# Kernel optimization log

Hardware: AMD Instinct MI355X
Metric: run time of the kernel (lower is better)

Reference implementation:

```python
import jax, jax.numpy as jnp
import numpy as np

# Mamba2(d_model=256, headdim=32) defaults: d_state=128, d_conv=4, expand=2, ngroups=1, chunk=256
B, CIN, L = 8, 256, 1024
D_MODEL = CIN
D_INNER = 2 * D_MODEL            # expand=2 -> 512
HEADDIM = 32
NHEADS = D_INNER // HEADDIM      # 16
D_STATE = 128
D_CONV = 4
CONV_DIM = D_INNER + 2 * D_STATE             # 768 (ngroups=1)
D_IN_PROJ = 2 * D_INNER + 2 * D_STATE + NHEADS  # 1296
GN_GROUPS = 8
CHUNK = 256
EPS = 1e-5

def setup_inputs():
    key = jax.random.key(0)
    ks = jax.random.split(key, 8)
    x = jax.random.normal(ks[0], (B, CIN, L), jnp.float32)
    W_in = jax.random.normal(ks[1], (D_IN_PROJ, D_MODEL), jnp.float32) * 0.02
    conv_w = jax.random.normal(ks[2], (CONV_DIM, D_CONV), jnp.float32) * 0.2
    conv_b = jax.random.normal(ks[3], (CONV_DIM,), jnp.float32) * 0.02
    dt = jnp.exp(jax.random.uniform(ks[4], (NHEADS,)) * (jnp.log(0.1) - jnp.log(0.001)) + jnp.log(0.001))
    dt_bias = dt + jnp.log(-jnp.expm1(-dt))   # inverse softplus
    A_log = jnp.log(jax.random.uniform(ks[5], (NHEADS,), minval=1.0, maxval=16.0))
    Dp = jnp.ones((NHEADS,), jnp.float32)
    rms_w = jnp.ones((D_INNER,), jnp.float32)
    W_out = jax.random.normal(ks[6], (D_MODEL, D_INNER), jnp.float32) * 0.02
    gn_w = jnp.ones((CIN,), jnp.float32)
    gn_b = jnp.zeros((CIN,), jnp.float32)
    return dict(x=x, W_in=W_in, conv_w=conv_w, conv_b=conv_b, dt_bias=dt_bias,
                A_log=A_log, Dp=Dp, rms_w=rms_w, W_out=W_out, gn_w=gn_w, gn_b=gn_b)

def segsum(a):
    # a: (..., T) -> (..., T, T) with sum_{j<i<=t} a_i on/below diagonal, -inf above
    T = a.shape[-1]
    cs = jnp.cumsum(a, -1)
    d = cs[..., :, None] - cs[..., None, :]
    mask = jnp.tril(jnp.ones((T, T), bool))
    return jnp.where(mask, d, -jnp.inf)

def ssd(X, A, Bm, Cm):
    # X: (b,l,h,p) already dt-scaled; A: (b,l,h) = dt*A_cont; Bm,Cm: (b,l,n) (ngroups=1)
    b, l, h, p = X.shape
    n = Bm.shape[-1]
    c = l // CHUNK
    X = X.reshape(b, c, CHUNK, h, p)
    A = A.reshape(b, c, CHUNK, h).transpose(0, 3, 1, 2)      # (b,h,c,l)
    Bm = Bm.reshape(b, c, CHUNK, n)
    Cm = Cm.reshape(b, c, CHUNK, n)
    A_cs = jnp.cumsum(A, -1)                                  # (b,h,c,l)
    Lmat = jnp.exp(segsum(A))                                 # (b,h,c,l,l)
    Y_diag = jnp.einsum('bcln,bcsn,bhcls,bcshp->bclhp', Cm, Bm, Lmat, X)
    decay_states = jnp.exp(A_cs[..., -1:] - A_cs)             # (b,h,c,l)
    states = jnp.einsum('bcln,bhcl,bclhp->bchpn', Bm, decay_states, X)
    decay_chunk = jnp.exp(segsum(jnp.pad(A_cs[..., -1], ((0, 0), (0, 0), (1, 0)))))  # (b,h,c+1,c+1)
    states = jnp.concatenate([jnp.zeros_like(states[:, :1]), states], axis=1)        # (b,c+1,h,p,n)
    prev = jnp.einsum('bhzc,bchpn->bzhpn', decay_chunk, states)[:, :-1]              # (b,c,h,p,n)
    Y_off = jnp.einsum('bcln,bchpn,bhcl->bclhp', Cm, prev, jnp.exp(A_cs))
    return (Y_diag + Y_off).reshape(b, l, h, p)

def _forward(x, W_in, conv_w, conv_b, dt_bias, A_log, Dp, rms_w, W_out, gn_w, gn_b):
    u = jnp.transpose(x, (0, 2, 1))                           # (B,L,d_model)
    zxbcdt = u @ W_in.T                                       # (B,L,1296)
    z = zxbcdt[..., :D_INNER]
    xBC = zxbcdt[..., D_INNER:D_INNER + CONV_DIM]
    dt = jax.nn.softplus(zxbcdt[..., D_INNER + CONV_DIM:] + dt_bias)  # (B,L,H)
    # causal depthwise conv1d + SiLU
    xpad = jnp.pad(xBC, ((0, 0), (D_CONV - 1, 0), (0, 0)))
    xconv = conv_b + sum(conv_w[:, k] * xpad[:, k:k + L, :] for k in range(D_CONV))
    xconv = jax.nn.silu(xconv)
    xs = xconv[..., :D_INNER].reshape(B, L, NHEADS, HEADDIM)
    Bm = xconv[..., D_INNER:D_INNER + D_STATE]
    Cm = xconv[..., D_INNER + D_STATE:]
    A = -jnp.exp(A_log)                                       # (H,)
    Y = ssd(dt[..., None] * xs, dt * A, Bm, Cm)               # (B,L,H,P)
    Y = Y + xs * Dp[None, None, :, None]
    # gated RMSNorm (norm_before_gate=False): rmsnorm(y * silu(z)) * weight
    y = Y.reshape(B, L, D_INNER) * jax.nn.silu(z)
    y = y * jax.lax.rsqrt(jnp.mean(y * y, -1, keepdims=True) + EPS) * rms_w
    out = jnp.transpose(y @ W_out.T, (0, 2, 1))               # (B,C,L)
    # GroupNorm(8, C) over (channels_per_group, L)
    og = out.reshape(B, GN_GROUPS, CIN // GN_GROUPS, L)
    mu = og.mean((2, 3), keepdims=True)
    var = og.var((2, 3), keepdims=True)
    out = ((og - mu) * jax.lax.rsqrt(var + EPS)).reshape(B, CIN, L)
    out = out * gn_w[None, :, None] + gn_b[None, :, None]
    return out * jnp.tanh(jax.nn.softplus(out))               # Mish

def reference(x, W_in, conv_w, conv_b, dt_bias, A_log, Dp, rms_w, W_out, gn_w, gn_b):
    return _forward(x, W_in, conv_w, conv_b, dt_bias, A_log, Dp, rms_w, W_out, gn_w, gn_b)
```

## Files before the change

kernel.cpp:

```cpp
#include <hip/hip_runtime.h>
#include <hip/hip_bf16.h>
#include <math.h>

#define B_ 8
#define L_ 1024
#define DM 256
#define DI 512
#define HD 32
#define NH 16
#define DS 128
#define CDIM 768
#define NZX 1280
#define CH 256
#define NC 4
#define M_ (B_*L_)
#define EPSV 1e-5f

typedef short bf16x8 __attribute__((ext_vector_type(8)));
typedef float f32x4 __attribute__((ext_vector_type(4)));

#define OFF_ZX   0
#define SZ_ZX    (M_*NZX/2)
#define OFF_XC   (OFF_ZX+SZ_ZX)
#define SZ_XC    (M_*CDIM/2)
#define OFF_DTP  (OFF_XC+SZ_XC)
#define SZ_DTP   (4*M_*NH)
#define OFF_ACS  (OFF_DTP+SZ_DTP)
#define SZ_ACS   (B_*NC*NH*CH)
#define OFF_S0   (OFF_ACS+SZ_ACS)
#define SZ_S0    (B_*NC*CH*CH/2)
#define OFF_ST   (OFF_S0+SZ_S0)
#define SZ_ST    (B_*NC*NH*HD*DS/2)
#define OFF_Y    (OFF_ST+SZ_ST)
#define SZ_Y     (M_*DI/2)
#define OFF_YNB  (OFF_Y+SZ_Y)
#define SZ_YNB   (M_*DI/2)
#define OFF_XBF  (OFF_YNB+SZ_YNB)
#define SZ_XBF   (M_*DM/2)
#define OFF_WBF  (OFF_XBF+SZ_XBF)
#define SZ_WBF   (1296*DM/2)
#define OFF_WOBF (OFF_WBF+SZ_WBF)
#define SZ_WOBF  (DM*DI/2)
#define OFF_GNP  (OFF_WOBF+SZ_WOBF)
#define SZ_GNP   (64*2)
#define OFF_BT   (OFF_GNP+SZ_GNP)
#define SZ_BT    (32*128*256/2)
#define OFF_OUTB (OFF_BT+SZ_BT)
#define SZ_OUTB  (M_*DM/2)

__device__ __forceinline__ ushort f2bf(float v) {
  __hip_bfloat16 h = __float2bfloat16(v);
  return *(ushort*)&h;
}
__device__ __forceinline__ float bf2f(ushort u) {
  return __uint_as_float(((unsigned int)u) << 16);
}
__device__ __forceinline__ float dt_load(const float* __restrict__ dtp, size_t di) {
  float s = dtp[di] + dtp[(size_t)M_*NH + di] + dtp[2*(size_t)M_*NH + di] + dtp[3*(size_t)M_*NH + di];
  return (s > 20.f) ? s : log1pf(expf(s));
}

__device__ __forceinline__ void gload16(const ushort* g, ushort* l) {
  __builtin_amdgcn_global_load_lds(
      (const __attribute__((address_space(1))) unsigned int*)g,
      (__attribute__((address_space(3))) unsigned int*)l,
      16, 0, 0);
}

__global__ __launch_bounds__(256) void k_prep(const float* __restrict__ x,
                                              const float* __restrict__ W_in,
                                              const float* __restrict__ W_out,
                                              const float* __restrict__ dt_bias,
                                              ushort* __restrict__ xbf,
                                              ushort* __restrict__ wbf,
                                              ushort* __restrict__ wobf,
                                              float2* __restrict__ gnp,
                                              float* __restrict__ dtp) {
  __shared__ float Ts[64][65];
  __shared__ float Wd[16][65];
  const int bid = blockIdx.x;
  const int t = threadIdx.x;
  if (bid < 512) {
    const int kt = bid & 3, lt2 = (bid >> 2) & 15, b = bid >> 6;
    const int k0 = kt*64, l0 = lt2*64;
    for (int i = t; i < 1024; i += 256) {
      int kk = i>>4, lw = i&15;
      float4 v = *(const float4*)&x[(size_t)b*DM*L_ + (size_t)(k0+kk)*L_ + l0 + lw*4];
      Ts[kk][lw*4+0] = v.x; Ts[kk][lw*4+1] = v.y;
      Ts[kk][lw*4+2] = v.z; Ts[kk][lw*4+3] = v.w;
    }
    for (int i = t; i < 1024; i += 256) {
      int h = i>>6, kk = i&63;
      Wd[h][kk] = W_in[(size_t)(NZX+h)*DM + k0+kk];
    }
    __syncthreads();
    for (int i = t; i < 512; i += 256) {
      int mm = i>>3, kg = i&7;
      union { ushort u[8]; uint4 q; } pk;
#pragma unroll
      for (int j = 0; j < 8; ++j) pk.u[j] = f2bf(Ts[kg*8+j][mm]);
      *(uint4*)&xbf[(size_t)(b*L_ + l0+mm)*DM + k0 + kg*8] = pk.q;
    }
    const int h = t&15, lg = t>>4;
    const float bias = (kt == 0) ? dt_bias[h] : 0.f;
#pragma unroll
    for (int c = 0; c < 4; ++c) {
      const int ll = lg + c*16;
      float acc = bias;
#pragma unroll 8
      for (int kk = 0; kk < 64; ++kk) acc += Wd[h][kk]*Ts[kk][ll];
      dtp[(size_t)kt*M_*NH + (size_t)(b*L_ + l0+ll)*NH + h] = acc;
    }
  } else if (bid < 512 + 1296) {
    int i = (bid-512)*256 + t;
    if (i < 1296*DM) wbf[i] = f2bf(W_in[i]);
  } else if (bid < 512 + 1296 + 512) {
    int i = (bid-512-1296)*256 + t;
    wobf[i] = f2bf(W_out[i]);
  } else {
    if (t < 64) gnp[t] = make_float2(0.f, 0.f);
  }
}

__global__ __launch_bounds__(256) void k_gemm_in_mfma(const ushort* __restrict__ xbf,
                                                      const ushort* __restrict__ wbf,
                                                      ushort* __restrict__ zxb) {
  __shared__ __attribute__((aligned(16))) ushort As[2][128*32];
  __shared__ __attribute__((aligned(16))) ushort Bs[2][128*32];
  const int tid = threadIdx.x;
  const int n0 = blockIdx.x*128, m0 = blockIdx.y*128;
  const int wave = tid>>6, lane = tid&63;
  const int lr = lane&15, quad = lane>>4;
  const int rA = lane>>2;
  const int cA = (lane&3)*8;
  f32x4 acc[2][8];
#pragma unroll
  for (int mi=0;mi<2;++mi)
#pragma unroll
    for (int ni=0;ni<8;++ni)
#pragma unroll
      for (int r=0;r<4;++r) acc[mi][ni][r] = 0.f;
  auto STAGE = [&](int buf, int k0) {
#pragma unroll
    for (int j = 0; j < 2; ++j) {
      const int ch = 2*wave + j;
      const int row = ch*16 + rA;
      gload16(xbf + (size_t)(m0+row)*DM + k0 + cA, &As[buf][ch*512]);
      gload16(wbf + (size_t)(n0+row)*DM + k0 + cA, &Bs[buf][ch*512]);
    }
  };
  STAGE(0, 0);
#pragma unroll
  for (int i = 0; i < 8; ++i) {
    __syncthreads();
    if (i < 7) STAGE((i+1)&1, (i+1)*32);
    const int cur = i&1;
    bf16x8 af[2], bfr[8];
    af[0] = *(const bf16x8*)&As[cur][(wave*32+lr)*32 + quad*8];
    af[1] = *(const bf16x8*)&As[cur][(wave*32+16+lr)*32 + quad*8];
#pragma unroll
    for (int ni=0;ni<8;++ni) bfr[ni] = *(const bf16x8*)&Bs[cur][(ni*16+lr)*32 + quad*8];
#pragma unroll
    for (int mi=0;mi<2;++mi)
#pragma unroll
      for (int ni=0;ni<8;++ni)
        acc[mi][ni] = __builtin_amdgcn_mfma_f32_16x16x32_bf16(af[mi], bfr[ni], acc[mi][ni], 0, 0, 0);
  }
#pragma unroll
  for (int mi=0;mi<2;++mi) {
    int m = m0 + wave*32 + mi*16 + quad*4;
#pragma unroll
    for (int ni=0;ni<8;++ni) {
      int n = n0 + ni*16 + lr;
#pragma unroll
      for (int r=0;r<4;++r) zxb[(size_t)(m+r)*NZX + n] = f2bf(acc[mi][ni][r]);
    }
  }
}

__global__ __launch_bounds__(256) void k_conv(const ushort* __restrict__ zxb,
                                              const float* __restrict__ cw,
                                              const float* __restrict__ cb,
                                              ushort* __restrict__ xcb,
                                              ushort* __restrict__ btg) {
  const int j = blockIdx.x*256 + threadIdx.x;
  const int m8 = blockIdx.y*8;
  const int l0 = m8 & 1023;
  const int mb = m8 & ~1023;
  const float4 w = *(const float4*)&cw[j*4];
  const float bias = cb[j];
  float v[11];
#pragma unroll
  for (int i = 0; i < 11; ++i) {
    int ll = l0 - 3 + i;
    v[i] = (ll >= 0) ? bf2f(zxb[(size_t)(mb+ll)*NZX + DI + j]) : 0.f;
  }
  union { ushort u[8]; uint4 q; } res;
#pragma unroll
  for (int i = 0; i < 8; ++i) {
    float a = bias + w.x*v[i] + w.y*v[i+1] + w.z*v[i+2] + w.w*v[i+3];
    a = a / (1.f + expf(-a));
    res.u[i] = f2bf(a);
    xcb[(size_t)(mb+l0+i)*CDIM + j] = res.u[i];
  }
  if (j >= DI && j < DI+DS) {
    const int n = j - DI;
    const int bc = (mb >> 10)*NC + (l0 >> 8);
    const int lc = l0 & 255;
    *(uint4*)&btg[((size_t)bc*DS + n)*CH + lc] = res.q;
  }
}

__global__ __launch_bounds__(256) void k_s0st(const ushort* __restrict__ xcb,
                                              const ushort* __restrict__ btg,
                                              const float* __restrict__ dtp,
                                              const float* __restrict__ A_log,
                                              float* __restrict__ acs_g,
                                              ushort* __restrict__ stb,
                                              ushort* __restrict__ S0b) {
  __shared__ float wtot[4];
  __shared__ ushort Xw[32][264];
  const int role = blockIdx.x;
  const int bc = blockIdx.y;
  const int base = bc*CH;
  const int t = threadIdx.x;
  const int wave = t>>6, lane = t&63, lr = lane&15, quad = lane>>4;
  if (role < 10) {
    const int lt = (role>=6) ? 3 : (role>=3) ? 2 : (role>=1) ? 1 : 0;
    const int st = role - lt*(lt+1)/2;
    const int l = lt*64 + wave*16 + lr;
    f32x4 acc[4];
#pragma unroll
    for (int nt = 0; nt < 4; ++nt)
#pragma unroll
      for (int r = 0; r < 4; ++r) acc[nt][r] = 0.f;
#pragma unroll
    for (int ks = 0; ks < 4; ++ks) {
      bf16x8 af = *(const bf16x8*)(xcb + (size_t)(base+l)*CDIM + (DI+DS) + ks*32 + quad*8);
#pragma unroll
      for (int nt = 0; nt < 4; ++nt) {
        bf16x8 bf = *(const bf16x8*)(xcb + (size_t)(base + st*64 + nt*16 + lr)*CDIM + DI + ks*32 + quad*8);
        acc[nt] = __builtin_amdgcn_mfma_f32_16x16x32_bf16(af, bf, acc[nt], 0, 0, 0);
      }
    }
    const bool diag = (lt == st);
#pragma unroll
    for (int nt = 0; nt < 4; ++nt)
#pragma unroll
      for (int r = 0; r < 4; ++r) {
        const int lrow = lt*64 + wave*16 + quad*4 + r;
        const int scol = st*64 + nt*16 + lr;
        ushort v = (!diag || scol <= lrow) ? f2bf(acc[nt][r]) : (ushort)0;
        S0b[((size_t)bc*CH + lrow)*CH + scol] = v;
      }
    return;
  }
  const int h = role - 10;
  float dt_t = dt_load(dtp, (size_t)(base+t)*NH + h);
  float An = -expf(A_log[h]);
  float v = dt_t * An;
#pragma unroll
  for (int off = 1; off < 64; off <<= 1) {
    float u = __shfl_up(v, off);
    if (lane >= off) v += u;
  }
  if (lane == 63) wtot[wave] = v;
  __syncthreads();
  float pre = 0.f, tot = 0.f;
#pragma unroll
  for (int wj = 0; wj < 4; ++wj) {
    float wv = wtot[wj];
    tot += wv;
    if (wj < wave) pre += wv;
  }
  const float a = v + pre;
  const float alast = tot;
  acs_g[((size_t)bc*NH + h)*CH + t] = a;
  float w = expf(alast - a) * dt_t;
  {
    const ushort* xp = xcb + (size_t)(base+t)*CDIM + h*HD;
    ushort tmp[32];
    *(uint4*)&tmp[0]  = *(const uint4*)(xp);
    *(uint4*)&tmp[8]  = *(const uint4*)(xp+8);
    *(uint4*)&tmp[16] = *(const uint4*)(xp+16);
    *(uint4*)&tmp[24] = *(const uint4*)(xp+24);
#pragma unroll
    for (int p = 0; p < 32; ++p) Xw[p][t] = f2bf(bf2f(tmp[p]) * w);
  }
  __syncthreads();
  f32x4 acc2[2][2];
#pragma unroll
  for (int mt=0;mt<2;++mt)
#pragma unroll
    for (int nt=0;nt<2;++nt)
#pragma unroll
      for (int r=0;r<4;++r) acc2[mt][nt][r] = 0.f;
  const ushort* bp = btg + (size_t)bc*DS*CH;
#pragma unroll
  for (int k0 = 0; k0 < CH; k0 += 32) {
    bf16x8 a0 = *(const bf16x8*)&Xw[lr][k0 + quad*8];
    bf16x8 a1 = *(const bf16x8*)&Xw[16+lr][k0 + quad*8];
    bf16x8 b0 = *(const bf16x8*)(bp + (size_t)(wave*32 + lr)*CH + k0 + quad*8);
    bf16x8 b1 = *(const bf16x8*)(bp + (size_t)(wave*32 + 16 + lr)*CH + k0 + quad*8);
    acc2[0][0] = __builtin_amdgcn_mfma_f32_16x16x32_bf16(a0, b0, acc2[0][0], 0,0,0);
    acc2[0][1] = __builtin_amdgcn_mfma_f32_16x16x32_bf16(a0, b1, acc2[0][1], 0,0,0);
    acc2[1][0] = __builtin_amdgcn_mfma_f32_16x16x32_bf16(a1, b0, acc2[1][0], 0,0,0);
    acc2[1][1] = __builtin_amdgcn_mfma_f32_16x16x32_bf16(a1, b1, acc2[1][1], 0,0,0);
  }
  size_t sb = ((size_t)bc*NH + h)*HD*DS;
#pragma unroll
  for (int mt = 0; mt < 2; ++mt)
#pragma unroll
    for (int nt = 0; nt < 2; ++nt)
#pragma unroll
      for (int r = 0; r < 4; ++r)
        stb[sb + (size_t)(mt*16 + quad*4 + r)*DS + wave*32 + nt*16 + lr] = f2bf(acc2[mt][nt][r]);
}

__global__ __launch_bounds__(256) void k_y_mfma(const ushort* __restrict__ xcb,
    const float* __restrict__ dtp, const float* __restrict__ acs_g,
    const ushort* __restrict__ S0b, const ushort* __restrict__ stb,
    const float* __restrict__ Dp, ushort* __restrict__ Yb) {
  __shared__ ushort Xt[32][280];
  __shared__ ushort Xs[32][280];
  __shared__ float acs[CH];
  const int t = threadIdx.x;
  const int bc = blockIdx.x, h = blockIdx.y;
  const int base = bc*CH;
  const int cc = bc & 3, bc4 = bc & ~3;
  acs[t] = acs_g[((size_t)bc*NH + h)*CH + t];
  const float dts_t = dt_load(dtp, (size_t)(base+t)*NH + h);
  ushort tmp[32];
  {
    const ushort* xp = xcb + (size_t)(base+t)*CDIM + h*HD;
    *(uint4*)&tmp[0]  = *(const uint4*)(xp);
    *(uint4*)&tmp[8]  = *(const uint4*)(xp+8);
    *(uint4*)&tmp[16] = *(const uint4*)(xp+16);
    *(uint4*)&tmp[24] = *(const uint4*)(xp+24);
#pragma unroll
    for (int p = 0; p < 32; ++p) Xt[p][t] = tmp[p];
  }
  __syncthreads();
  const float e32 = expf(acs[t & ~31] - acs[t]) * dts_t;
#pragma unroll
  for (int p = 0; p < 32; ++p) Xs[p][t] = f2bf(bf2f(tmp[p]) * e32);
  __syncthreads();
  const int wave = t>>6, lane = t&63, lr = lane&15, quad = lane>>4;
  f32x4 acc[4][2];
#pragma unroll
  for (int mt=0;mt<4;++mt)
#pragma unroll
    for (int nt=0;nt<2;++nt)
#pragma unroll
      for (int r=0;r<4;++r) acc[mt][nt][r] = 0.f;
  if (cc > 0) {
    float fj[3];
    {
      float cum = 0.f;
      for (int j = cc-1; j >= 0; --j) {
        fj[j] = expf(cum);
        cum += acs_g[((size_t)(bc4+j)*NH + h)*CH + (CH-1)];
      }
    }
#pragma unroll
    for (int ks = 0; ks < 4; ++ks) {
      bf16x8 bfr[2];
#pragma unroll
      for (int nt = 0; nt < 2; ++nt) {
        float P[8];
#pragma unroll
        for (int jj = 0; jj < 8; ++jj) P[jj] = 0.f;
        for (int j = 0; j < cc; ++j) {
          bf16x8 sv = *(const bf16x8*)(stb + ((size_t)(bc4+j)*NH + h)*HD*DS
                                       + (size_t)(nt*16+lr)*DS + ks*32 + quad*8);
#pragma unroll
          for (int jj = 0; jj < 8; ++jj) P[jj] += fj[j]*bf2f((ushort)sv[jj]);
        }
        bf16x8 bb;
#pragma unroll
        for (int jj = 0; jj < 8; ++jj) bb[jj] = (short)f2bf(P[jj]);
        bfr[nt] = bb;
      }
#pragma unroll
      for (int mt = 0; mt < 4; ++mt) {
        int l = mt*64 + wave*16 + lr;
        bf16x8 af = *(const bf16x8*)(xcb + (size_t)(base+l)*CDIM + (DI+DS) + ks*32 + quad*8);
        acc[mt][0] = __builtin_amdgcn_mfma_f32_16x16x32_bf16(af, bfr[0], acc[mt][0], 0,0,0);
        acc[mt][1] = __builtin_amdgcn_mfma_f32_16x16x32_bf16(af, bfr[1], acc[mt][1], 0,0,0);
      }
    }
    const float es0 = expf(acs[0]);
#pragma unroll
    for (int mt = 0; mt < 4; ++mt)
#pragma unroll
      for (int nt = 0; nt < 2; ++nt)
#pragma unroll
        for (int r = 0; r < 4; ++r) acc[mt][nt][r] *= es0;
  }
  const int Kw = (12 + wave) >> 1;
  for (int ks = 0; ks <= Kw; ++ks) {
    const int sq = ks*32;
    const bf16x8 xb0 = *(const bf16x8*)&Xs[lr][sq + quad*8];
    const bf16x8 xb1 = *(const bf16x8*)&Xs[16+lr][sq + quad*8];
    const float g = (ks > 0) ? expf(acs[sq] - acs[sq-32]) : 1.f;
#pragma unroll
    for (int mt = 0; mt < 4; ++mt) {
      const int rt = 4*mt + wave;
      if (ks > (rt>>1)) continue;
      if (ks > 0) {
#pragma unroll
        for (int r = 0; r < 4; ++r) { acc[mt][0][r] *= g; acc[mt][1][r] *= g; }
      }
      const int l = mt*64 + wave*16 + lr;
      const bf16x8 sb = *(const bf16x8*)(S0b + ((size_t)bc*CH + l)*CH + sq + quad*8);
      acc[mt][0] = __builtin_amdgcn_mfma_f32_16x16x32_bf16(sb, xb0, acc[mt][0], 0,0,0);
      acc[mt][1] = __builtin_amdgcn_mfma_f32_16x16x32_bf16(sb, xb1, acc[mt][1], 0,0,0);
    }
  }
  const float dph = Dp[h];
#pragma unroll
  for (int mt = 0; mt < 4; ++mt) {
    const int Kmt = (4*mt + wave) >> 1;
    const float aref = acs[32*Kmt];
    const int lb = mt*64 + wave*16 + quad*4;
#pragma unroll
    for (int r = 0; r < 4; ++r) {
      const float e = expf(acs[lb+r] - aref);
#pragma unroll
      for (int nt = 0; nt < 2; ++nt) {
        const int p = nt*16 + lr;
        float xv = bf2f(Xt[p][lb+r]);
        Yb[(size_t)(base+lb+r)*DI + h*HD + p] = f2bf(acc[mt][nt][r]*e + dph*xv);
      }
    }
  }
}

__global__ __launch_bounds__(256) void k_rms(const ushort* __restrict__ zxb,
                                             const ushort* __restrict__ Yb,
                                             const float* __restrict__ rw,
                                             ushort* __restrict__ yn) {
  const int m = blockIdx.x*4 + (threadIdx.x>>6);
  const int lane = threadIdx.x & 63;
  const int c0 = lane*8;
  bf16x8 zv = *(const bf16x8*)(zxb + (size_t)m*NZX + c0);
  bf16x8 yv = *(const bf16x8*)(Yb  + (size_t)m*DI  + c0);
  float y[8];
  float ss = 0.f;
#pragma unroll
  for (int j = 0; j < 8; ++j) {
    float z = bf2f((ushort)zv[j]);
    y[j] = bf2f((ushort)yv[j]) * z / (1.f + expf(-z));
    ss += y[j]*y[j];
  }
#pragma unroll
  for (int off = 1; off < 64; off <<= 1) ss += __shfl_xor(ss, off);
  const float inv = rsqrtf(ss * (1.f/DI) + EPSV);
  float4 w0 = *(const float4*)&rw[c0];
  float4 w1 = *(const float4*)&rw[c0+4];
  const float wv[8] = {w0.x,w0.y,w0.z,w0.w,w1.x,w1.y,w1.z,w1.w};
  union { ushort u[8]; uint4 q; } pk;
#pragma unroll
  for (int j = 0; j < 8; ++j) pk.u[j] = f2bf(y[j] * inv * wv[j]);
  *(uint4*)(yn + (size_t)m*DI + c0) = pk.q;
}

__global__ __launch_bounds__(256) void k_gemm_out_mfma(const ushort* __restrict__ ynbf,
                                                       const ushort* __restrict__ wobf,
                                                       ushort* __restrict__ outb,
                                                       float2* __restrict__ gnp) {
  __shared__ __attribute__((aligned(16))) ushort As[2][64*32];
  __shared__ __attribute__((aligned(16))) ushort Bs[2][128*32];
  __shared__ float red[4][8];
  const int tid = threadIdx.x;
  const int n0 = blockIdx.x*128, m0 = blockIdx.y*64;
  const int wave = tid>>6, lane = tid&63;
  const int lr = lane&15, quad = lane>>4;
  const int rA = lane>>2;
  const int cA = (lane&3)*8;
  f32x4 acc[8];
#pragma unroll
  for (int ni=0;ni<8;++ni)
#pragma unroll
    for (int r=0;r<4;++r) acc[ni][r] = 0.f;
  auto STAGE = [&](int buf, int k0) {
    gload16(ynbf + (size_t)(m0 + wave*16 + rA)*DI + k0 + cA, &As[buf][wave*512]);
#pragma unroll
    for (int j = 0; j < 2; ++j) {
      const int ch = 2*wave + j;
      gload16(wobf + (size_t)(n0 + ch*16 + rA)*DI + k0 + cA, &Bs[buf][ch*512]);
    }
  };
  STAGE(0, 0);
#pragma unroll
  for (int i = 0; i < 16; ++i) {
    __syncthreads();
    if (i < 15) STAGE((i+1)&1, (i+1)*32);
    const int cur = i&1;
    bf16x8 af = *(const bf16x8*)&As[cur][(wave*16+lr)*32 + quad*8];
    bf16x8 bfr[8];
#pragma unroll
    for (int ni=0;ni<8;++ni) bfr[ni] = *(const bf16x8*)&Bs[cur][(ni*16+lr)*32 + quad*8];
#pragma unroll
    for (int ni=0;ni<8;++ni)
      acc[ni] = __builtin_amdgcn_mfma_f32_16x16x32_bf16(af, bfr[ni], acc[ni], 0, 0, 0);
  }
  const int b = m0 >> 10, l0 = m0 & 1023;
  float sg[4] = {0.f,0.f,0.f,0.f}, sq2[4] = {0.f,0.f,0.f,0.f};
#pragma unroll
  for (int ni=0;ni<8;++ni) {
    int n = n0 + ni*16 + lr;
    union { ushort u[4]; uint2 q; } pk;
#pragma unroll
    for (int r=0;r<4;++r) pk.u[r] = f2bf(acc[ni][r]);
    *(uint2*)&outb[(size_t)b*DM*L_ + (size_t)n*L_ + l0 + wave*16 + quad*4] = pk.q;
    float ps = acc[ni][0]+acc[ni][1]+acc[ni][2]+acc[ni][3];
    float pq = acc[ni][0]*acc[ni][0]+acc[ni][1]*acc[ni][1]
             + acc[ni][2]*acc[ni][2]+acc[ni][3]*acc[ni][3];
    sg[ni>>1] += ps; sq2[ni>>1] += pq;
  }
#pragma unroll
  for (int g = 0; g < 4; ++g)
#pragma unroll
    for (int off = 32; off > 0; off >>= 1) {
      sg[g]  += __shfl_down(sg[g],  off);
      sq2[g] += __shfl_down(sq2[g], off);
    }
  if (lane == 0) {
#pragma unroll
    for (int g = 0; g < 4; ++g) { red[wave][g] = sg[g]; red[wave][4+g] = sq2[g]; }
  }
  __syncthreads();
  if (tid == 0) {
    int g0 = b*8 + (n0>>5);
#pragma unroll
    for (int g = 0; g < 4; ++g) {
      float S = red[0][g]+red[1][g]+red[2][g]+red[3][g];
      float Q = red[0][4+g]+red[1][4+g]+red[2][4+g]+red[3][4+g];
      atomicAdd(&gnp[g0+g].x, S);
      atomicAdd(&gnp[g0+g].y, Q);
    }
  }
}

__global__ __launch_bounds__(256) void k_gn_apply(const float2* __restrict__ gnp,
                                                  const float* __restrict__ gw,
                                                  const float* __restrict__ gb,
                                                  const ushort* __restrict__ ob,
                                                  float* __restrict__ o) {
  const int ch = blockIdx.x & 255, b = blockIdx.x >> 8;
  const int t = threadIdx.x;
  float2 p = gnp[b*8 + (ch>>5)];
  const float mean = p.x * (1.f/(32.f*L_));
  const float var  = p.y * (1.f/(32.f*L_)) - mean*mean;
  const float inv  = rsqrtf(var + EPSV);
  const float w = gw[ch], bb = gb[ch];
  size_t base = (size_t)blockIdx.x * L_;
  ushort4 v = *(const ushort4*)&ob[base + t*4];
  float r[4] = {bf2f(v.x), bf2f(v.y), bf2f(v.z), bf2f(v.w)};
#pragma unroll
  for (int j = 0; j < 4; ++j) {
    float u = (r[j] - mean) * inv * w + bb;
    float m;
    if (u > 15.f) m = u;
    else {
      float e = expf(u);
      float a = 1.f + e;
      float a2 = a*a;
      m = u * (a2 - 1.f) / (a2 + 1.f);
    }
    r[j] = m;
  }
  *(float4*)&o[base + t*4] = make_float4(r[0], r[1], r[2], r[3]);
}

extern "C" void kernel_launch(void* const* d_in, const int* in_sizes, int n_in,
                              void* d_out, int out_size, void* d_ws, size_t ws_size,
                              hipStream_t stream) {
  const float* x       = (const float*)d_in[0];
  const float* W_in    = (const float*)d_in[1];
  const float* conv_w  = (const float*)d_in[2];
  const float* conv_b  = (const float*)d_in[3];
  const float* dt_bias = (const float*)d_in[4];
  const float* A_log   = (const float*)d_in[5];
  const float* Dp      = (const float*)d_in[6];
  const float* rms_w   = (const float*)d_in[7];
  const float* W_out   = (const float*)d_in[8];
  const float* gn_w    = (const float*)d_in[9];
  const float* gn_b    = (const float*)d_in[10];
  float* out = (float*)d_out;
  float* ws  = (float*)d_ws;

  ushort* zxb   = (ushort*)(ws + OFF_ZX);
  ushort* xcb   = (ushort*)(ws + OFF_XC);
  float*  dtp   = ws + OFF_DTP;
  float*  acs   = ws + OFF_ACS;
  ushort* S0b   = (ushort*)(ws + OFF_S0);
  ushort* stb   = (ushort*)(ws + OFF_ST);
  ushort* Ybb   = (ushort*)(ws + OFF_Y);
  ushort* ynbf  = (ushort*)(ws + OFF_YNB);
  ushort* xbf   = (ushort*)(ws + OFF_XBF);
  ushort* wbf   = (ushort*)(ws + OFF_WBF);
  ushort* wobf  = (ushort*)(ws + OFF_WOBF);
  float2* gnp   = (float2*)(ws + OFF_GNP);
  ushort* btg   = (ushort*)(ws + OFF_BT);
  ushort* outb  = (ushort*)(ws + OFF_OUTB);

  k_prep         <<<dim3(512+1296+512+1), 256, 0, stream>>>(x, W_in, W_out, dt_bias,
                                                            xbf, wbf, wobf, gnp, dtp);
  k_gemm_in_mfma <<<dim3(NZX/128, M_/128), 256, 0, stream>>>(xbf, wbf, zxb);
  k_conv         <<<dim3(3, M_/8), 256, 0, stream>>>(zxb, conv_w, conv_b, xcb, btg);
  k_s0st         <<<dim3(26, B_*NC), 256, 0, stream>>>(xcb, btg, dtp, A_log, acs, stb, S0b);
  k_y_mfma       <<<dim3(B_*NC, NH), 256, 0, stream>>>(xcb, dtp, acs, S0b, stb, Dp, Ybb);
  k_rms          <<<dim3(M_/4), 256, 0, stream>>>(zxb, Ybb, rms_w, ynbf);
  k_gemm_out_mfma<<<dim3(DM/128, M_/64), 256, 0, stream>>>(ynbf, wobf, outb, gnp);
  k_gn_apply     <<<dim3(B_*DM), 256, 0, stream>>>(gnp, gn_w, gn_b, outb, out);
}
```

Baseline: 176.0 us.

## Fuse GroupNorm+Mish apply into output GEMM via grid-wide barrier

Removes the separate GroupNorm/Mish kernel and runs its work inside the output GEMM kernel after a software grid barrier (atomic counter spin). The barrier counter is reset in the prep kernel. This drops one kernel launch and its tail gap. The cost is a spin barrier that relies on all 256 blocks being co-resident, which is not guaranteed by the launch and could deadlock. Outputs written by other blocks are also read back without explicit cache invalidation beyond acquire semantics.

After: 189.6 us. 7.7% more time.

```diff
diff --git a/kernel.cpp b/kernel.cpp
--- a/kernel.cpp
+++ b/kernel.cpp
@@ -15,6 +15,7 @@
 #define NC 4
 #define M_ (B_*L_)
 #define EPSV 1e-5f
+#define OUTGRID 256
 
 typedef short bf16x8 __attribute__((ext_vector_type(8)));
 typedef float f32x4 __attribute__((ext_vector_type(4)));
@@ -47,6 +48,7 @@
 #define SZ_BT    (32*128*256/2)
 #define OFF_OUTB (OFF_BT+SZ_BT)
 #define SZ_OUTB  (M_*DM/2)
+#define OFF_BAR  (OFF_OUTB+SZ_OUTB)
 
 __device__ __forceinline__ ushort f2bf(float v) {
   __hip_bfloat16 h = __float2bfloat16(v);
@@ -65,6 +67,16 @@
       (const __attribute__((address_space(1))) unsigned int*)g,
       (__attribute__((address_space(3))) unsigned int*)l,
       16, 0, 0);
+}
+
+__device__ __forceinline__ void gbar(int* ctr) {
+  __syncthreads();
+  if (threadIdx.x == 0) {
+    __hip_atomic_fetch_add(ctr, 1, __ATOMIC_ACQ_REL, __HIP_MEMORY_SCOPE_AGENT);
+    while (__hip_atomic_load(ctr, __ATOMIC_ACQUIRE, __HIP_MEMORY_SCOPE_AGENT) < OUTGRID)
+      __builtin_amdgcn_s_sleep(2);
+  }
+  __syncthreads();
 }
 
 __global__ __launch_bounds__(256) void k_prep(const float* __restrict__ x,
@@ -75,7 +87,8 @@
                                               ushort* __restrict__ wbf,
                                               ushort* __restrict__ wobf,
                                               float2* __restrict__ gnp,
-                                              float* __restrict__ dtp) {
+                                              float* __restrict__ dtp,
+                                              int* __restrict__ bar) {
   __shared__ float Ts[64][65];
   __shared__ float Wd[16][65];
   const int bid = blockIdx.x;
@@ -119,6 +132,7 @@
     wobf[i] = f2bf(W_out[i]);
   } else {
     if (t < 64) gnp[t] = make_float2(0.f, 0.f);
+    if (t == 64) bar[0] = 0;
   }
 }
 
@@ -467,8 +481,12 @@
 
 __global__ __launch_bounds__(256) void k_gemm_out_mfma(const ushort* __restrict__ ynbf,
                                                        const ushort* __restrict__ wobf,
+                                                       const float* __restrict__ gw,
+                                                       const float* __restrict__ gbb,
                                                        ushort* __restrict__ outb,
-                                                       float2* __restrict__ gnp) {
+                                                       float2* __restrict__ gnp,
+                                                       float* __restrict__ o,
+                                                       int* __restrict__ bar) {
   __shared__ __attribute__((aligned(16))) ushort As[2][64*32];
   __shared__ __attribute__((aligned(16))) ushort Bs[2][128*32];
   __shared__ float red[4][8];
@@ -541,37 +559,35 @@
       atomicAdd(&gnp[g0+g].y, Q);
     }
   }
-}
-
-__global__ __launch_bounds__(256) void k_gn_apply(const float2* __restrict__ gnp,
-                                                  const float* __restrict__ gw,
-                                                  const float* __restrict__ gb,
-                                                  const ushort* __restrict__ ob,
-                                                  float* __restrict__ o) {
-  const int ch = blockIdx.x & 255, b = blockIdx.x >> 8;
-  const int t = threadIdx.x;
-  float2 p = gnp[b*8 + (ch>>5)];
-  const float mean = p.x * (1.f/(32.f*L_));
-  const float var  = p.y * (1.f/(32.f*L_)) - mean*mean;
-  const float inv  = rsqrtf(var + EPSV);
-  const float w = gw[ch], bb = gb[ch];
-  size_t base = (size_t)blockIdx.x * L_;
-  ushort4 v = *(const ushort4*)&ob[base + t*4];
-  float r[4] = {bf2f(v.x), bf2f(v.y), bf2f(v.z), bf2f(v.w)};
-#pragma unroll
-  for (int j = 0; j < 4; ++j) {
-    float u = (r[j] - mean) * inv * w + bb;
-    float m;
-    if (u > 15.f) m = u;
-    else {
-      float e = expf(u);
-      float a = 1.f + e;
-      float a2 = a*a;
-      m = u * (a2 - 1.f) / (a2 + 1.f);
-    }
-    r[j] = m;
-  }
-  *(float4*)&o[base + t*4] = make_float4(r[0], r[1], r[2], r[3]);
+  gbar(bar);
+  const int bid = blockIdx.x + 2*blockIdx.y;
+#pragma unroll
+  for (int r = 0; r < 8; ++r) {
+    const int g = bid*8 + r;
+    const int ch = g & 255, bb2 = g >> 8;
+    float2 p = gnp[bb2*8 + (ch>>5)];
+    const float mean = p.x * (1.f/(32.f*L_));
+    const float var  = p.y * (1.f/(32.f*L_)) - mean*mean;
+    const float inv  = rsqrtf(var + EPSV);
+    const float w = gw[ch], bg = gbb[ch];
+    size_t base2 = (size_t)g * L_;
+    ushort4 v = *(const ushort4*)&outb[base2 + tid*4];
+    float rr[4] = {bf2f(v.x), bf2f(v.y), bf2f(v.z), bf2f(v.w)};
+#pragma unroll
+    for (int j = 0; j < 4; ++j) {
+      float u = (rr[j] - mean) * inv * w + bg;
+      float m;
+      if (u > 15.f) m = u;
+      else {
+        float e = expf(u);
+        float a = 1.f + e;
+        float a2 = a*a;
+        m = u * (a2 - 1.f) / (a2 + 1.f);
+      }
+      rr[j] = m;
+    }
+    *(float4*)&o[base2 + tid*4] = make_float4(rr[0], rr[1], rr[2], rr[3]);
+  }
 }
 
 extern "C" void kernel_launch(void* const* d_in, const int* in_sizes, int n_in,
@@ -605,14 +621,15 @@
   float2* gnp   = (float2*)(ws + OFF_GNP);
   ushort* btg   = (ushort*)(ws + OFF_BT);
   ushort* outb  = (ushort*)(ws + OFF_OUTB);
+  int*    bar   = (int*)(ws + OFF_BAR);
 
   k_prep         <<<dim3(512+1296+512+1), 256, 0, stream>>>(x, W_in, W_out, dt_bias,
-                                                            xbf, wbf, wobf, gnp, dtp);
+                                                            xbf, wbf, wobf, gnp, dtp, bar);
   k_gemm_in_mfma <<<dim3(NZX/128, M_/128), 256, 0, stream>>>(xbf, wbf, zxb);
   k_conv         <<<dim3(3, M_/8), 256, 0, stream>>>(zxb, conv_w, conv_b, xcb, btg);
   k_s0st         <<<dim3(26, B_*NC), 256, 0, stream>>>(xcb, btg, dtp, A_log, acs, stb, S0b);
   k_y_mfma       <<<dim3(B_*NC, NH), 256, 0, stream>>>(xcb, dtp, acs, S0b, stb, Dp, Ybb);
   k_rms          <<<dim3(M_/4), 256, 0, stream>>>(zxb, Ybb, rms_w, ynbf);
-  k_gemm_out_mfma<<<dim3(DM/128, M_/64), 256, 0, stream>>>(ynbf, wobf, outb, gnp);
-  k_gn_apply     <<<dim3(B_*DM), 256, 0, stream>>>(gnp, gn_w, gn_b, outb, out);
-}
+  k_gemm_out_mfma<<<dim3(DM/128, M_/64), 256, 0, stream>>>(ynbf, wobf, gn_w, gn_b,
+                                                           outb, gnp, out, bar);
+}
```

## Remap block indices so each batch stays on one XCD's L2

Applied to the files above, without the earlier changes.

Every kernel now flattens its grid to 1D and decodes the batch index from the low three bits of the block id. Round-robin dispatch across the eight XCDs should then keep each batch's intermediates in one XCD's L2 from kernel to kernel. The aim is fewer L2 misses and less cross-die traffic. The risk is that it depends on the dispatch order and changes the order in which tiles are visited.

After: 176.2 us. Within noise of the previous version (+0.1%).

```diff
diff --git a/kernel.cpp b/kernel.cpp
--- a/kernel.cpp
+++ b/kernel.cpp
@@ -81,7 +81,8 @@
   const int bid = blockIdx.x;
   const int t = threadIdx.x;
   if (bid < 512) {
-    const int kt = bid & 3, lt2 = (bid >> 2) & 15, b = bid >> 6;
+    const int b = bid & 7, rest = bid >> 3;
+    const int kt = rest & 3, lt2 = rest >> 2;
     const int k0 = kt*64, l0 = lt2*64;
     for (int i = t; i < 1024; i += 256) {
       int kk = i>>4, lw = i&15;
@@ -128,7 +129,9 @@
   __shared__ __attribute__((aligned(16))) ushort As[2][128*32];
   __shared__ __attribute__((aligned(16))) ushort Bs[2][128*32];
   const int tid = threadIdx.x;
-  const int n0 = blockIdx.x*128, m0 = blockIdx.y*128;
+  const int id = blockIdx.x;
+  const int b = id & 7, r8 = id >> 3;
+  const int m0 = (b*8 + r8/10)*128, n0 = (r8%10)*128;
   const int wave = tid>>6, lane = tid&63;
   const int lr = lane&15, quad = lane>>4;
   const int rA = lane>>2;
@@ -183,10 +186,11 @@
                                               const float* __restrict__ cb,
                                               ushort* __restrict__ xcb,
                                               ushort* __restrict__ btg) {
-  const int j = blockIdx.x*256 + threadIdx.x;
-  const int m8 = blockIdx.y*8;
-  const int l0 = m8 & 1023;
-  const int mb = m8 & ~1023;
+  const int id = blockIdx.x;
+  const int b = id & 7, r8 = id >> 3;
+  const int j = (r8%3)*256 + threadIdx.x;
+  const int l0 = (r8/3)*8;
+  const int mb = b*1024;
   const float4 w = *(const float4*)&cw[j*4];
   const float bias = cb[j];
   float v[11];
@@ -205,7 +209,7 @@
   }
   if (j >= DI && j < DI+DS) {
     const int n = j - DI;
-    const int bc = (mb >> 10)*NC + (l0 >> 8);
+    const int bc = b*NC + (l0 >> 8);
     const int lc = l0 & 255;
     *(uint4*)&btg[((size_t)bc*DS + n)*CH + lc] = res.q;
   }
@@ -220,8 +224,10 @@
                                               ushort* __restrict__ S0b) {
   __shared__ float wtot[4];
   __shared__ ushort Xw[32][264];
-  const int role = blockIdx.x;
-  const int bc = blockIdx.y;
+  const int id = blockIdx.x;
+  const int b = id & 7, r8 = id >> 3;
+  const int role = r8 % 26;
+  const int bc = b*NC + r8/26;
   const int base = bc*CH;
   const int t = threadIdx.x;
   const int wave = t>>6, lane = t&63, lr = lane&15, quad = lane>>4;
@@ -325,7 +331,10 @@
   __shared__ ushort Xs[32][280];
   __shared__ float acs[CH];
   const int t = threadIdx.x;
-  const int bc = blockIdx.x, h = blockIdx.y;
+  const int id = blockIdx.x;
+  const int b = id & 7, r8 = id >> 3;
+  const int h = r8 % 16;
+  const int bc = b*NC + r8/16;
   const int base = bc*CH;
   const int cc = bc & 3, bc4 = bc & ~3;
   acs[t] = acs_g[((size_t)bc*NH + h)*CH + t];
@@ -440,7 +449,9 @@
                                              const ushort* __restrict__ Yb,
                                              const float* __restrict__ rw,
                                              ushort* __restrict__ yn) {
-  const int m = blockIdx.x*4 + (threadIdx.x>>6);
+  const int id = blockIdx.x;
+  const int b = id & 7, r8 = id >> 3;
+  const int m = b*1024 + r8*4 + (threadIdx.x>>6);
   const int lane = threadIdx.x & 63;
   const int c0 = lane*8;
   bf16x8 zv = *(const bf16x8*)(zxb + (size_t)m*NZX + c0);
@@ -473,7 +484,9 @@
   __shared__ __attribute__((aligned(16))) ushort Bs[2][128*32];
   __shared__ float red[4][8];
   const int tid = threadIdx.x;
-  const int n0 = blockIdx.x*128, m0 = blockIdx.y*64;
+  const int id = blockIdx.x;
+  const int b = id & 7, r8 = id >> 3;
+  const int m0 = b*1024 + (r8>>1)*64, n0 = (r8&1)*128;
   const int wave = tid>>6, lane = tid&63;
   const int lr = lane&15, quad = lane>>4;
   const int rA = lane>>2;
@@ -505,7 +518,7 @@
     for (int ni=0;ni<8;++ni)
       acc[ni] = __builtin_amdgcn_mfma_f32_16x16x32_bf16(af, bfr[ni], acc[ni], 0, 0, 0);
   }
-  const int b = m0 >> 10, l0 = m0 & 1023;
+  const int l0 = m0 & 1023;
   float sg[4] = {0.f,0.f,0.f,0.f}, sq2[4] = {0.f,0.f,0.f,0.f};
 #pragma unroll
   for (int ni=0;ni<8;++ni) {
@@ -548,14 +561,15 @@
                                                   const float* __restrict__ gb,
                                                   const ushort* __restrict__ ob,
                                                   float* __restrict__ o) {
-  const int ch = blockIdx.x & 255, b = blockIdx.x >> 8;
+  const int id = blockIdx.x;
+  const int b = id & 7, ch = id >> 3;
   const int t = threadIdx.x;
   float2 p = gnp[b*8 + (ch>>5)];
   const float mean = p.x * (1.f/(32.f*L_));
   const float var  = p.y * (1.f/(32.f*L_)) - mean*mean;
   const float inv  = rsqrtf(var + EPSV);
   const float w = gw[ch], bb = gb[ch];
-  size_t base = (size_t)blockIdx.x * L_;
+  size_t base = ((size_t)b*DM + ch) * L_;
   ushort4 v = *(const ushort4*)&ob[base + t*4];
   float r[4] = {bf2f(v.x), bf2f(v.y), bf2f(v.z), bf2f(v.w)};
 #pragma unroll
@@ -608,11 +622,11 @@
 
   k_prep         <<<dim3(512+1296+512+1), 256, 0, stream>>>(x, W_in, W_out, dt_bias,
                                                             xbf, wbf, wobf, gnp, dtp);
-  k_gemm_in_mfma <<<dim3(NZX/128, M_/128), 256, 0, stream>>>(xbf, wbf, zxb);
-  k_conv         <<<dim3(3, M_/8), 256, 0, stream>>>(zxb, conv_w, conv_b, xcb, btg);
-  k_s0st         <<<dim3(26, B_*NC), 256, 0, stream>>>(xcb, btg, dtp, A_log, acs, stb, S0b);
-  k_y_mfma       <<<dim3(B_*NC, NH), 256, 0, stream>>>(xcb, dtp, acs, S0b, stb, Dp, Ybb);
-  k_rms          <<<dim3(M_/4), 256, 0, stream>>>(zxb, Ybb, rms_w, ynbf);
-  k_gemm_out_mfma<<<dim3(DM/128, M_/64), 256, 0, stream>>>(ynbf, wobf, outb, gnp);
-  k_gn_apply     <<<dim3(B_*DM), 256, 0, stream>>>(gnp, gn_w, gn_b, outb, out);
-}
+  k_gemm_in_mfma <<<dim3(640),  256, 0, stream>>>(xbf, wbf, zxb);
+  k_conv         <<<dim3(3072), 256, 0, stream>>>(zxb, conv_w, conv_b, xcb, btg);
+  k_s0st         <<<dim3(832),  256, 0, stream>>>(xcb, btg, dtp, A_log, acs, stb, S0b);
+  k_y_mfma       <<<dim3(512),  256, 0, stream>>>(xcb, dtp, acs, S0b, stb, Dp, Ybb);
+  k_rms          <<<dim3(2048), 256, 0, stream>>>(zxb, Ybb, rms_w, ynbf);
+  k_gemm_out_mfma<<<dim3(256),  256, 0, stream>>>(ynbf, wobf, outb, gnp);
+  k_gn_apply     <<<dim3(2048), 256, 0, stream>>>(gnp, gn_w, gn_b, outb, out);
+}
```
